# Performance work log

Measured on AMD Instinct MI355X. Metric: run time of the kernel, lower is better.

The kernel has to match this reference:

```python
import jax, jax.numpy as jnp
import numpy as np

L, B, N, IN, H, ATTN, RED, OUT = 3, 8, 512, 64, 128, 32, 32, 3


def setup_inputs() -> dict:
    key = jax.random.key(0)
    ks = jax.random.split(key, 34)
    def rn(i, shape, s=0.05):
        return jax.random.normal(ks[i], shape, dtype=jnp.float32) * s
    inp = {
        "X": rn(0, (B, N, IN), 1.0),
        # sparse binary adjacency (avg degree ~10) and denser clique graph
        "A": (jax.random.uniform(ks[1], (B, N, N)) < 0.02).astype(jnp.float32),
        "Ac": (jax.random.uniform(ks[2], (B, N, N)) < 0.05).astype(jnp.float32),
        # topo embedding
        "embed_w": rn(3, (H, IN)), "embed_b": jnp.zeros((H,), jnp.float32),
        "topo_eps": jnp.zeros((1,), jnp.float32),
        "topo_w": rn(4, (H, H)), "topo_b": jnp.zeros((H,), jnp.float32),
        "theta": rn(5, (H, 2)),
        # per-layer dual GIN (index 0: A, index 1: Ac)
        "gin_eps": jnp.zeros((L, 2, 1), jnp.float32),
        "gin_w": rn(6, (L, 2, H, H)), "gin_b": jnp.zeros((L, 2, H), jnp.float32),
        # per-layer flexible attention
        "wo": rn(7, (L, ATTN, H)), "w1": rn(8, (L, ATTN, H)),
        "wphi": rn(9, (L, ATTN)),
        "wy_w": rn(10, (L, H, H)), "wy_b": jnp.zeros((L, H), jnp.float32),
        "we_w": rn(11, (L, H, ATTN)), "we_b": jnp.zeros((L, H), jnp.float32),
        # per-layer SE block
        "lin1_w": rn(12, (L, RED, H)), "lin1_b": jnp.zeros((L, RED), jnp.float32),
        "lin2_w": rn(13, (L, H, RED)), "lin2_b": jnp.zeros((L, H), jnp.float32),
        "mlp_w": rn(14, (L, H, H)), "mlp_b": jnp.zeros((L, H), jnp.float32),
        # node head
        "head1_w": rn(15, (H // 2, H)), "head1_b": jnp.zeros((H // 2,), jnp.float32),
        "head2_w": rn(16, (OUT, H // 2)), "head2_b": jnp.zeros((OUT,), jnp.float32),
    }
    return inp


def _lin(x, w, b=None):
    y = x @ w.T
    return y if b is None else y + b


def _gin(x, a, eps, w, b):
    # (1+eps)*X + A@X, then Linear, then ReLU
    return jax.nn.relu(_lin((1.0 + eps) * x + a @ x, w, b))


def _forward(X, A, Ac, embed_w, embed_b, topo_eps, topo_w, topo_b, theta,
             gin_eps, gin_w, gin_b, wo, w1, wphi, wy_w, wy_b, we_w, we_b,
             lin1_w, lin1_b, lin2_w, lin2_b, mlp_w, mlp_b,
             head1_w, head1_b, head2_w, head2_b):
    # TopoPositionalEmbedding (shared GIN on both graphs)
    Xh = _lin(X, embed_w, embed_b)                      # (B,N,H)
    hA = _gin(Xh, A, topo_eps[0], topo_w, topo_b)
    hAC = _gin(Xh, Ac, topo_eps[0], topo_w, topo_b)
    Xp = Xh + jnp.tanh(hA * theta[:, 0]) + jnp.tanh(hAC * theta[:, 1])

    for l in range(L):
        # dual GIN
        XA = _gin(Xp, A, gin_eps[l, 0, 0], gin_w[l, 0], gin_b[l, 0])
        XAC = _gin(Xp, Ac, gin_eps[l, 1, 0], gin_w[l, 1], gin_b[l, 1])
        # GRIT-style flexible attention
        ho = Xp @ wo[l].T                               # (B,N,ATTN)
        h1 = Xp @ w1[l].T
        e = jnp.tanh(ho[:, :, None, :] + h1[:, None, :, :])   # (B,N,N,ATTN)
        alpha = jax.nn.softmax(e @ wphi[l], axis=-1)    # (B,N,N)
        Xy = _lin(Xp, wy_w[l], wy_b[l])                 # (B,N,H)
        # sum_j alpha_ij * We(e_ij) == We(sum_j alpha_ij * e_ij) since We is affine
        # and sum_j alpha_ij == 1 (avoids the (B,N,N,H) intermediate)
        ctx = jnp.einsum('bij,bijd->bid', alpha, e)     # (B,N,ATTN)
        Xatt = alpha @ Xy + _lin(ctx, we_w[l], we_b[l])
        Xbar = XA + XAC + Xatt
        # SE gating
        y1 = jax.nn.relu(_lin(Xbar.sum(axis=1), lin1_w[l], lin1_b[l]))
        y2 = jax.nn.sigmoid(_lin(y1, lin2_w[l], lin2_b[l]))
        Xp = _lin(Xbar * y2[:, None, :], mlp_w[l], mlp_b[l])

    h = jax.nn.relu(_lin(Xp, head1_w, head1_b))
    return _lin(h, head2_w, head2_b)                    # (B,N,OUT)


def reference(X, A, Ac, embed_w, embed_b, topo_eps, topo_w, topo_b, theta,
              gin_eps, gin_w, gin_b, wo, w1, wphi, wy_w, wy_b, we_w, we_b,
              lin1_w, lin1_b, lin2_w, lin2_b, mlp_w, mlp_b,
              head1_w, head1_b, head2_w, head2_b):
    return _forward(X, A, Ac, embed_w, embed_b, topo_eps, topo_w, topo_b, theta,
                    gin_eps, gin_w, gin_b, wo, w1, wphi, wy_w, wy_b, we_w, we_b,
                    lin1_w, lin1_b, lin2_w, lin2_b, mlp_w, mlp_b,
                    head1_w, head1_b, head2_w, head2_b)
```

## Files before the change

kernel.cpp:

```cpp
#include <hip/hip_runtime.h>

#define Bc 8
#define Nc 512
#define INc 64
#define Hc 128
#define Atc 32
#define REDc 32
#define OUTc 3
#define Lc 3
#define MNc (Bc * Nc)

__device__ __forceinline__ float tanh_fast(float x) {
    float e = __expf(2.f * x);
    return 1.f - 2.f * __builtin_amdgcn_rcpf(e + 1.f);
}

template <int TM, int K, int ACT>
__global__ __launch_bounds__(256) void gemm256(
        const float* __restrict__ X, const float* __restrict__ W,
        const float* __restrict__ bias, float* __restrict__ Y,
        const float* __restrict__ scale) {
    constexpr int RPG = TM / 2;
    __shared__ float xs[TM * K];
    int m0 = blockIdx.x * TM;
    int t = threadIdx.x;
    const float* sc = scale ? scale + (size_t)(m0 >> 9) * K : nullptr;
    for (int idx4 = t; idx4 < TM * K / 4; idx4 += 256) {
        float4 v = ((const float4*)(X + (size_t)m0 * K))[idx4];
        if (sc) {
            int base = idx4 * 4;
            v.x *= sc[base & (K - 1)]; v.y *= sc[(base + 1) & (K - 1)];
            v.z *= sc[(base + 2) & (K - 1)]; v.w *= sc[(base + 3) & (K - 1)];
        }
        ((float4*)xs)[idx4] = v;
    }
    __syncthreads();
    int n = t & 127;
    int grp = t >> 7;
    float bv = bias ? bias[n] : 0.f;
    float acc[RPG];
#pragma unroll
    for (int r = 0; r < RPG; ++r) acc[r] = bv;
    const float* w = W + (size_t)n * K;
    for (int k = 0; k < K; k += 4) {
        float4 wv = *(const float4*)(w + k);
#pragma unroll
        for (int r = 0; r < RPG; ++r) {
            float4 xv = *(const float4*)(xs + (grp * RPG + r) * K + k);
            acc[r] = fmaf(xv.x, wv.x, acc[r]); acc[r] = fmaf(xv.y, wv.y, acc[r]);
            acc[r] = fmaf(xv.z, wv.z, acc[r]); acc[r] = fmaf(xv.w, wv.w, acc[r]);
        }
    }
#pragma unroll
    for (int r = 0; r < RPG; ++r) {
        float v = acc[r];
        if (ACT) v = fmaxf(v, 0.f);
        Y[(size_t)(m0 + grp * RPG + r) * 128 + n] = v;
    }
}

__global__ __launch_bounds__(128) void build_csr(
        const float* __restrict__ A, const float* __restrict__ Acg,
        int* __restrict__ idxA, int* __restrict__ idxC,
        int* __restrict__ cntA, int* __restrict__ cntC) {
    int bi = blockIdx.x;
    int h = threadIdx.x;
    __shared__ int cA, cC;
    if (h == 0) { cA = 0; cC = 0; }
    __syncthreads();
    int* ia = idxA + (size_t)bi * Nc;
    int* ic = idxC + (size_t)bi * Nc;
    {
        float4 a4 = ((const float4*)(A + (size_t)bi * Nc))[h];
        if (a4.x != 0.f) ia[atomicAdd(&cA, 1)] = 4 * h;
        if (a4.y != 0.f) ia[atomicAdd(&cA, 1)] = 4 * h + 1;
        if (a4.z != 0.f) ia[atomicAdd(&cA, 1)] = 4 * h + 2;
        if (a4.w != 0.f) ia[atomicAdd(&cA, 1)] = 4 * h + 3;
        float4 c4 = ((const float4*)(Acg + (size_t)bi * Nc))[h];
        if (c4.x != 0.f) ic[atomicAdd(&cC, 1)] = 4 * h;
        if (c4.y != 0.f) ic[atomicAdd(&cC, 1)] = 4 * h + 1;
        if (c4.z != 0.f) ic[atomicAdd(&cC, 1)] = 4 * h + 2;
        if (c4.w != 0.f) ic[atomicAdd(&cC, 1)] = 4 * h + 3;
    }
    __syncthreads();
    if (h == 0) { cntA[bi] = cA; cntC[bi] = cC; }
}

__global__ __launch_bounds__(128) void spmm_pre(
        const int* __restrict__ idxA, const int* __restrict__ idxC,
        const int* __restrict__ cntA, const int* __restrict__ cntC,
        const float* __restrict__ X, const float* __restrict__ eA,
        const float* __restrict__ eC, float* __restrict__ T1, float* __restrict__ T2) {
    int bi = blockIdx.x;
    int b = bi >> 9;
    int h = threadIdx.x;
    __shared__ int ias[Nc], ics[Nc];
    int nA = cntA[bi], nC = cntC[bi];
    for (int q = h; q < nA; q += 128) ias[q] = idxA[(size_t)bi * Nc + q];
    for (int q = h; q < nC; q += 128) ics[q] = idxC[(size_t)bi * Nc + q];
    __syncthreads();
    const float* Xb = X + (size_t)b * Nc * Hc;
    float a1 = 0.f, a2 = 0.f;
    for (int q = 0; q < nA; ++q) a1 += Xb[(size_t)ias[q] * Hc + h];
    for (int q = 0; q < nC; ++q) a2 += Xb[(size_t)ics[q] * Hc + h];
    size_t o = (size_t)bi * Hc + h;
    float xv = X[o];
    T1[o] = (1.f + eA[0]) * xv + a1;
    T2[o] = (1.f + eC[0]) * xv + a2;
}

__global__ __launch_bounds__(256) void gemm2_topo(
        const float* __restrict__ T1, const float* __restrict__ T2,
        const float* __restrict__ W, const float* __restrict__ bias,
        const float* __restrict__ Xh, const float* __restrict__ theta,
        float* __restrict__ Xp) {
    __shared__ float xs1[8 * Hc], xs2[8 * Hc];
    int m0 = blockIdx.x * 8;
    int t = threadIdx.x;
    for (int idx4 = t; idx4 < 8 * Hc / 4; idx4 += 256) {
        ((float4*)xs1)[idx4] = ((const float4*)(T1 + (size_t)m0 * Hc))[idx4];
        ((float4*)xs2)[idx4] = ((const float4*)(T2 + (size_t)m0 * Hc))[idx4];
    }
    __syncthreads();
    int n = t & 127, grp = t >> 7;
    float bv = bias[n];
    float ac1[4], ac2[4];
#pragma unroll
    for (int r = 0; r < 4; ++r) { ac1[r] = bv; ac2[r] = bv; }
    const float* w = W + (size_t)n * Hc;
    for (int k = 0; k < Hc; k += 4) {
        float4 wv = *(const float4*)(w + k);
#pragma unroll
        for (int r = 0; r < 4; ++r) {
            float4 x1 = *(const float4*)(xs1 + (grp * 4 + r) * Hc + k);
            float4 x2 = *(const float4*)(xs2 + (grp * 4 + r) * Hc + k);
            ac1[r] = fmaf(x1.x, wv.x, ac1[r]); ac1[r] = fmaf(x1.y, wv.y, ac1[r]);
            ac1[r] = fmaf(x1.z, wv.z, ac1[r]); ac1[r] = fmaf(x1.w, wv.w, ac1[r]);
            ac2[r] = fmaf(x2.x, wv.x, ac2[r]); ac2[r] = fmaf(x2.y, wv.y, ac2[r]);
            ac2[r] = fmaf(x2.z, wv.z, ac2[r]); ac2[r] = fmaf(x2.w, wv.w, ac2[r]);
        }
    }
    float th0 = theta[2 * n], th1 = theta[2 * n + 1];
#pragma unroll
    for (int r = 0; r < 4; ++r) {
        size_t o = (size_t)(m0 + grp * 4 + r) * Hc + n;
        float g1 = fmaxf(ac1[r], 0.f), g2 = fmaxf(ac2[r], 0.f);
        Xp[o] = Xh[o] + tanh_fast(g1 * th0) + tanh_fast(g2 * th1);
    }
}

__global__ __launch_bounds__(256) void layer_gemms(
        const float* __restrict__ T1, const float* __restrict__ T2,
        const float* __restrict__ W1, const float* __restrict__ b1,
        const float* __restrict__ W2, const float* __restrict__ b2,
        const float* __restrict__ Xp, const float* __restrict__ wy_w,
        const float* __restrict__ wy_b, const float* __restrict__ wo,
        const float* __restrict__ w1a, float* __restrict__ GS,
        float* __restrict__ Xy, float* __restrict__ hov, float* __restrict__ h1v) {
    __shared__ float xs1[8 * Hc], xs2[8 * Hc], xs[8 * Hc];
    int m0 = blockIdx.x * 8;
    int t = threadIdx.x;
    for (int idx4 = t; idx4 < 8 * Hc / 4; idx4 += 256) {
        ((float4*)xs1)[idx4] = ((const float4*)(T1 + (size_t)m0 * Hc))[idx4];
        ((float4*)xs2)[idx4] = ((const float4*)(T2 + (size_t)m0 * Hc))[idx4];
        ((float4*)xs)[idx4]  = ((const float4*)(Xp + (size_t)m0 * Hc))[idx4];
    }
    __syncthreads();
    int n = t & 127, grp = t >> 7;
    {
        float ac1[4], ac2[4];
        float bv1 = b1[n], bv2 = b2[n];
#pragma unroll
        for (int r = 0; r < 4; ++r) { ac1[r] = bv1; ac2[r] = bv2; }
        const float* w1 = W1 + (size_t)n * Hc;
        const float* w2 = W2 + (size_t)n * Hc;
        for (int k = 0; k < Hc; k += 4) {
            float4 wv1 = *(const float4*)(w1 + k);
            float4 wv2 = *(const float4*)(w2 + k);
#pragma unroll
            for (int r = 0; r < 4; ++r) {
                float4 x1 = *(const float4*)(xs1 + (grp * 4 + r) * Hc + k);
                float4 x2 = *(const float4*)(xs2 + (grp * 4 + r) * Hc + k);
                ac1[r] = fmaf(x1.x, wv1.x, ac1[r]); ac1[r] = fmaf(x1.y, wv1.y, ac1[r]);
                ac1[r] = fmaf(x1.z, wv1.z, ac1[r]); ac1[r] = fmaf(x1.w, wv1.w, ac1[r]);
                ac2[r] = fmaf(x2.x, wv2.x, ac2[r]); ac2[r] = fmaf(x2.y, wv2.y, ac2[r]);
                ac2[r] = fmaf(x2.z, wv2.z, ac2[r]); ac2[r] = fmaf(x2.w, wv2.w, ac2[r]);
            }
        }
#pragma unroll
        for (int r = 0; r < 4; ++r) {
            size_t o = (size_t)(m0 + grp * 4 + r) * Hc + n;
            GS[o] = fmaxf(ac1[r], 0.f) + fmaxf(ac2[r], 0.f);
        }
    }
    {
        float bv = wy_b[n];
        float acc[4];
#pragma unroll
        for (int r = 0; r < 4; ++r) acc[r] = bv;
        const float* w = wy_w + (size_t)n * Hc;
        for (int k = 0; k < Hc; k += 4) {
            float4 wv = *(const float4*)(w + k);
#pragma unroll
            for (int r = 0; r < 4; ++r) {
                float4 xv = *(const float4*)(xs + (grp * 4 + r) * Hc + k);
                acc[r] = fmaf(xv.x, wv.x, acc[r]); acc[r] = fmaf(xv.y, wv.y, acc[r]);
                acc[r] = fmaf(xv.z, wv.z, acc[r]); acc[r] = fmaf(xv.w, wv.w, acc[r]);
            }
        }
#pragma unroll
        for (int r = 0; r < 4; ++r)
            Xy[(size_t)(m0 + grp * 4 + r) * Hc + n] = acc[r];
    }
    {
        int n2 = t & 63, g2 = t >> 6;
        const float* w = (n2 < 32) ? (wo + (size_t)n2 * Hc) : (w1a + (size_t)(n2 - 32) * Hc);
        float acc[2] = {0.f, 0.f};
        for (int k = 0; k < Hc; k += 4) {
            float4 wv = *(const float4*)(w + k);
#pragma unroll
            for (int r = 0; r < 2; ++r) {
                float4 xv = *(const float4*)(xs + (g2 * 2 + r) * Hc + k);
                acc[r] = fmaf(xv.x, wv.x, acc[r]); acc[r] = fmaf(xv.y, wv.y, acc[r]);
                acc[r] = fmaf(xv.z, wv.z, acc[r]); acc[r] = fmaf(xv.w, wv.w, acc[r]);
            }
        }
#pragma unroll
        for (int r = 0; r < 2; ++r) {
            int m = m0 + g2 * 2 + r;
            float v = tanh_fast(acc[r]);
            if (n2 < 32) hov[(size_t)m * Atc + n2] = v;
            else h1v[(size_t)m * Atc + (n2 - 32)] = v;
        }
    }
}

__global__ __launch_bounds__(256, 4) void attn_part(
        const float* __restrict__ ta, const float* __restrict__ tb,
        const float* __restrict__ wphi, const float* __restrict__ Xy,
        float* __restrict__ Pp, float* __restrict__ ctxp, float* __restrict__ wsp) {
    int blk = blockIdx.x;
    int b = blk >> 8;
    int r6 = (blk >> 2) & 63;
    int js = blk & 3;
    int i0 = r6 * 8;
    int t = threadIdx.x;
    __shared__ float als[8 * 128];
    __shared__ float4 red4[1024];
    __shared__ float tas[8 * 32];
    tas[t] = ta[((size_t)b * Nc + i0) * 32 + t];
    __syncthreads();
    {
        int i = t >> 5;
        int kq = t & 3;
        int jl = (t >> 2) & 7;
        float4 wp0 = ((const float4*)wphi)[kq * 2];
        float4 wp1 = ((const float4*)wphi)[kq * 2 + 1];
        float4 ta0 = *(const float4*)(tas + i * 32 + kq * 8);
        float4 ta1 = *(const float4*)(tas + i * 32 + kq * 8 + 4);
        const float* tbb = tb + ((size_t)b * Nc + js * 128) * 32;
        const float4* p = (const float4*)(tbb + (size_t)jl * 32 + kq * 8);
        float4 c0a = p[0], c0b = p[1];
        float4 c1a = p[64], c1b = p[65];
        float ca[8];
#pragma unroll
        for (int q = 0; q < 8; ++q) ca[q] = 0.f;
        float wsum = 0.f;
#pragma unroll 4
        for (int jj = 0; jj < 16; ++jj) {
            float4 ha = c0a, hb = c0b;
            c0a = c1a; c0b = c1b;
            if (jj < 14) { c1a = p[(jj + 2) * 64]; c1b = p[(jj + 2) * 64 + 1]; }
            float e0 = (ta0.x + ha.x) * __builtin_amdgcn_rcpf(fmaf(ta0.x, ha.x, 1.f));
            float e1 = (ta0.y + ha.y) * __builtin_amdgcn_rcpf(fmaf(ta0.y, ha.y, 1.f));
            float e2 = (ta0.z + ha.z) * __builtin_amdgcn_rcpf(fmaf(ta0.z, ha.z, 1.f));
            float e3 = (ta0.w + ha.w) * __builtin_amdgcn_rcpf(fmaf(ta0.w, ha.w, 1.f));
            float e4 = (ta1.x + hb.x) * __builtin_amdgcn_rcpf(fmaf(ta1.x, hb.x, 1.f));
            float e5 = (ta1.y + hb.y) * __builtin_amdgcn_rcpf(fmaf(ta1.y, hb.y, 1.f));
            float e6 = (ta1.z + hb.z) * __builtin_amdgcn_rcpf(fmaf(ta1.z, hb.z, 1.f));
            float e7 = (ta1.w + hb.w) * __builtin_amdgcn_rcpf(fmaf(ta1.w, hb.w, 1.f));
            float s01 = fmaf(e1, wp0.y, e0 * wp0.x);
            float s23 = fmaf(e3, wp0.w, e2 * wp0.z);
            float s45 = fmaf(e5, wp1.y, e4 * wp1.x);
            float s67 = fmaf(e7, wp1.w, e6 * wp1.z);
            float sc = (s01 + s23) + (s45 + s67);
            sc += __shfl_xor(sc, 1);
            sc += __shfl_xor(sc, 2);
            float w = __expf(sc);
            if (kq == 0) als[i * 128 + jj * 8 + jl] = w;
            wsum += w;
            ca[0] = fmaf(w, e0, ca[0]);
            ca[1] = fmaf(w, e1, ca[1]);
            ca[2] = fmaf(w, e2, ca[2]);
            ca[3] = fmaf(w, e3, ca[3]);
            ca[4] = fmaf(w, e4, ca[4]);
            ca[5] = fmaf(w, e5, ca[5]);
            ca[6] = fmaf(w, e6, ca[6]);
            ca[7] = fmaf(w, e7, ca[7]);
        }
#pragma unroll
        for (int o = 16; o > 0; o >>= 1) wsum += __shfl_xor(wsum, o);
        if ((t & 31) == 0) wsp[(size_t)js * MNc + (size_t)b * Nc + i0 + i] = wsum;
#pragma unroll
        for (int q = 0; q < 8; ++q) {
            ca[q] += __shfl_xor(ca[q], 4);
            ca[q] += __shfl_xor(ca[q], 8);
            ca[q] += __shfl_xor(ca[q], 16);
        }
        if (jl == 0) {
            float* cp = ctxp + ((size_t)js * MNc + (size_t)b * Nc + i0 + i) * 32 + kq * 8;
#pragma unroll
            for (int q = 0; q < 8; ++q) cp[q] = ca[q];
        }
    }
    __syncthreads();
    {
        int h4 = t & 31, jg = t >> 5;
        const float* xp = Xy + (((size_t)b * Nc + js * 128) + jg * 16) * Hc + h4 * 4;
        float* Pb = Pp + (size_t)js * MNc * Hc;
        float4 acc[8];
#pragma unroll
        for (int r = 0; r < 8; ++r) acc[r] = make_float4(0.f, 0.f, 0.f, 0.f);
        float4 xc = *(const float4*)(xp);
        float4 xn = *(const float4*)(xp + Hc);
#pragma unroll 4
        for (int jq = 0; jq < 16; ++jq) {
            float4 x = xc;
            xc = xn;
            if (jq < 14) xn = *(const float4*)(xp + (jq + 2) * Hc);
            int j = jg * 16 + jq;
#pragma unroll
            for (int r = 0; r < 8; ++r) {
                float av = als[r * 128 + j];
                acc[r].x = fmaf(av, x.x, acc[r].x);
                acc[r].y = fmaf(av, x.y, acc[r].y);
                acc[r].z = fmaf(av, x.z, acc[r].z);
                acc[r].w = fmaf(av, x.w, acc[r].w);
            }
        }
#pragma unroll
        for (int r = 0; r < 4; ++r) red4[jg * 128 + r * 32 + h4] = acc[r];
        __syncthreads();
        if (t < 128) {
            int ii = t >> 5, hq = t & 31;
            float4 s = red4[ii * 32 + hq];
#pragma unroll
            for (int gq = 1; gq < 8; ++gq) {
                float4 p = red4[gq * 128 + ii * 32 + hq];
                s.x += p.x; s.y += p.y; s.z += p.z; s.w += p.w;
            }
            *(float4*)(Pb + ((size_t)b * Nc + i0 + ii) * Hc + hq * 4) = s;
        }
        __syncthreads();
#pragma unroll
        for (int r = 0; r < 4; ++r) red4[jg * 128 + r * 32 + h4] = acc[4 + r];
        __syncthreads();
        if (t < 128) {
            int ii = t >> 5, hq = t & 31;
            float4 s = red4[ii * 32 + hq];
#pragma unroll
            for (int gq = 1; gq < 8; ++gq) {
                float4 p = red4[gq * 128 + ii * 32 + hq];
                s.x += p.x; s.y += p.y; s.z += p.z; s.w += p.w;
            }
            *(float4*)(Pb + ((size_t)b * Nc + i0 + 4 + ii) * Hc + hq * 4) = s;
        }
    }
}

__global__ __launch_bounds__(256) void combine_se(
        const float* __restrict__ Pp, const float* __restrict__ ctxp,
        const float* __restrict__ wsp, const float* __restrict__ we_w,
        const float* __restrict__ we_b, const float* __restrict__ GS,
        float* __restrict__ Xbar, float* __restrict__ part) {
    int blk = blockIdx.x;
    int m0 = blk * 8;
    int t = threadIdx.x;
    __shared__ float ctxs[8 * 32];
    __shared__ float sinv[8];
    __shared__ float4 sred[256];
    if (t < 8) {
        float ws = 0.f;
#pragma unroll
        for (int s = 0; s < 4; ++s) ws += wsp[(size_t)s * MNc + m0 + t];
        sinv[t] = 4.f / ws;
    }
    {
        float c = 0.f;
#pragma unroll
        for (int s = 0; s < 4; ++s) c += ctxp[((size_t)s * MNc + m0) * 32 + t];
        ctxs[t] = c;
    }
    __syncthreads();
    int ii = t >> 5, hq = t & 31;
    size_t o = (size_t)(m0 + ii) * Hc + hq * 4;
    float4 ps = *(const float4*)(Pp + o);
#pragma unroll
    for (int s = 1; s < 4; ++s) {
        float4 p = *(const float4*)(Pp + (size_t)s * MNc * Hc + o);
        ps.x += p.x; ps.y += p.y; ps.z += p.z; ps.w += p.w;
    }
    float si = sinv[ii];
    const float* c = ctxs + ii * 32;
    float wec[4];
#pragma unroll
    for (int ho_ = 0; ho_ < 4; ++ho_) {
        const float4* wrow = (const float4*)(we_w + (size_t)(hq * 4 + ho_) * 32);
        float sv = 0.f;
#pragma unroll
        for (int q = 0; q < 8; ++q) {
            float4 w4 = wrow[q];
            sv = fmaf(w4.x, c[4 * q], sv); sv = fmaf(w4.y, c[4 * q + 1], sv);
            sv = fmaf(w4.z, c[4 * q + 2], sv); sv = fmaf(w4.w, c[4 * q + 3], sv);
        }
        wec[ho_] = sv;
    }
    float4 wb = *(const float4*)(we_b + hq * 4);
    float4 gv = *(const float4*)(GS + o);
    float4 outv;
    outv.x = (ps.x + wec[0]) * si + wb.x + gv.x;
    outv.y = (ps.y + wec[1]) * si + wb.y + gv.y;
    outv.z = (ps.z + wec[2]) * si + wb.z + gv.z;
    outv.w = (ps.w + wec[3]) * si + wb.w + gv.w;
    *(float4*)(Xbar + o) = outv;
    sred[ii * 32 + hq] = outv;
    __syncthreads();
    if (t < 32) {
        float4 s0 = sred[t];
#pragma unroll
        for (int g = 1; g < 8; ++g) {
            float4 p = sred[g * 32 + t];
            s0.x += p.x; s0.y += p.y; s0.z += p.z; s0.w += p.w;
        }
        *(float4*)(part + (size_t)blk * Hc + t * 4) = s0;
    }
}

__global__ __launch_bounds__(256) void mlp_gemm(
        const float* __restrict__ Xbar, const float* __restrict__ W,
        const float* __restrict__ bias, const float* __restrict__ part,
        const float* __restrict__ l1w, const float* __restrict__ l1b,
        const float* __restrict__ l2w, const float* __restrict__ l2b,
        float* __restrict__ Y) {
    __shared__ float xs[8 * Hc];
    __shared__ float s[Hc];
    __shared__ float y1s[REDc];
    __shared__ float y2s[Hc];
    int m0 = blockIdx.x * 8;
    int b = m0 >> 9;
    int t = threadIdx.x;
    ((float4*)xs)[t] = ((const float4*)(Xbar + (size_t)m0 * Hc))[t];
    if (t < 128) {
        const float* pb = part + (size_t)b * 64 * Hc;
        float acc = 0.f;
        for (int p = 0; p < 64; ++p) acc += pb[p * Hc + t];
        s[t] = acc;
    }
    __syncthreads();
    if (t < REDc) {
        float a = l1b[t];
        const float* w = l1w + (size_t)t * Hc;
        for (int k = 0; k < Hc; ++k) a = fmaf(s[k], w[k], a);
        y1s[t] = fmaxf(a, 0.f);
    }
    __syncthreads();
    if (t < 128) {
        float a = l2b[t];
        const float* w2 = l2w + (size_t)t * REDc;
#pragma unroll
        for (int k = 0; k < REDc; ++k) a = fmaf(y1s[k], w2[k], a);
        y2s[t] = 1.f / (1.f + __expf(-a));
    }
    __syncthreads();
    {
        float4 yv = ((const float4*)y2s)[t & 31];
        float4 v = ((float4*)xs)[t];
        v.x *= yv.x; v.y *= yv.y; v.z *= yv.z; v.w *= yv.w;
        ((float4*)xs)[t] = v;
    }
    __syncthreads();
    int n = t & 127, grp = t >> 7;
    float bv = bias[n];
    float acc[4];
#pragma unroll
    for (int r = 0; r < 4; ++r) acc[r] = bv;
    const float* w = W + (size_t)n * Hc;
    for (int k = 0; k < Hc; k += 4) {
        float4 wv = *(const float4*)(w + k);
#pragma unroll
        for (int r = 0; r < 4; ++r) {
            float4 xv = *(const float4*)(xs + (grp * 4 + r) * Hc + k);
            acc[r] = fmaf(xv.x, wv.x, acc[r]); acc[r] = fmaf(xv.y, wv.y, acc[r]);
            acc[r] = fmaf(xv.z, wv.z, acc[r]); acc[r] = fmaf(xv.w, wv.w, acc[r]);
        }
    }
#pragma unroll
    for (int r = 0; r < 4; ++r)
        Y[(size_t)(m0 + grp * 4 + r) * Hc + n] = acc[r];
}

__global__ __launch_bounds__(256) void head_kernel(
        const float* __restrict__ Xp, const float* __restrict__ h1w,
        const float* __restrict__ h1b, const float* __restrict__ h2w,
        const float* __restrict__ h2b, float* __restrict__ out) {
    __shared__ float xs[8 * Hc];
    __shared__ float hs[8 * 64];
    int m0 = blockIdx.x * 8;
    int t = threadIdx.x;
    ((float4*)xs)[t] = ((const float4*)(Xp + (size_t)m0 * Hc))[t];
    __syncthreads();
    {
        int n = t & 63, grp = t >> 6;
        float a0 = h1b[n], a1 = a0;
        const float* w = h1w + (size_t)n * Hc;
        const float* x0 = xs + (grp * 2) * Hc;
        const float* x1 = xs + (grp * 2 + 1) * Hc;
        for (int k = 0; k < Hc; k += 4) {
            float4 wv = *(const float4*)(w + k);
            float4 v0 = *(const float4*)(x0 + k);
            float4 v1 = *(const float4*)(x1 + k);
            a0 = fmaf(v0.x, wv.x, a0); a0 = fmaf(v0.y, wv.y, a0);
            a0 = fmaf(v0.z, wv.z, a0); a0 = fmaf(v0.w, wv.w, a0);
            a1 = fmaf(v1.x, wv.x, a1); a1 = fmaf(v1.y, wv.y, a1);
            a1 = fmaf(v1.z, wv.z, a1); a1 = fmaf(v1.w, wv.w, a1);
        }
        hs[(grp * 2) * 64 + n] = fmaxf(a0, 0.f);
        hs[(grp * 2 + 1) * 64 + n] = fmaxf(a1, 0.f);
    }
    __syncthreads();
    if (t < 8 * OUTc) {
        int m = t / OUTc, o = t - m * OUTc;
        float a = h2b[o];
        const float* w2 = h2w + (size_t)o * 64;
        const float* hr = hs + m * 64;
#pragma unroll
        for (int k = 0; k < 64; ++k) a = fmaf(hr[k], w2[k], a);
        out[(size_t)(m0 + m) * OUTc + o] = a;
    }
}

extern "C" void kernel_launch(void* const* d_in, const int* in_sizes, int n_in,
                              void* d_out, int out_size, void* d_ws, size_t ws_size,
                              hipStream_t stream) {
    const float* X       = (const float*)d_in[0];
    const float* A       = (const float*)d_in[1];
    const float* Acg     = (const float*)d_in[2];
    const float* embed_w = (const float*)d_in[3];
    const float* embed_b = (const float*)d_in[4];
    const float* topo_eps= (const float*)d_in[5];
    const float* topo_w  = (const float*)d_in[6];
    const float* topo_b  = (const float*)d_in[7];
    const float* theta   = (const float*)d_in[8];
    const float* gin_eps = (const float*)d_in[9];
    const float* gin_w   = (const float*)d_in[10];
    const float* gin_b   = (const float*)d_in[11];
    const float* wo      = (const float*)d_in[12];
    const float* w1      = (const float*)d_in[13];
    const float* wphi    = (const float*)d_in[14];
    const float* wy_w    = (const float*)d_in[15];
    const float* wy_b    = (const float*)d_in[16];
    const float* we_w    = (const float*)d_in[17];
    const float* we_b    = (const float*)d_in[18];
    const float* lin1_w  = (const float*)d_in[19];
    const float* lin1_b  = (const float*)d_in[20];
    const float* lin2_w  = (const float*)d_in[21];
    const float* lin2_b  = (const float*)d_in[22];
    const float* mlp_w   = (const float*)d_in[23];
    const float* mlp_b   = (const float*)d_in[24];
    const float* head1_w = (const float*)d_in[25];
    const float* head1_b = (const float*)d_in[26];
    const float* head2_w = (const float*)d_in[27];
    const float* head2_b = (const float*)d_in[28];
    float* out = (float*)d_out;

    float* ws = (float*)d_ws;
    const int MN = Bc * Nc;
    const size_t SZ = (size_t)MN * Hc;
    float* Xh   = ws;
    float* Xp   = Xh + SZ;
    float* T1   = Xp + SZ;
    float* T2   = T1 + SZ;
    float* GS   = T2 + SZ;
    float* Xy   = GS + SZ;
    float* hov  = Xy + SZ;
    float* h1v  = hov + (size_t)MN * Atc;
    float* part = h1v + (size_t)MN * Atc;
    float* Pp   = part + (size_t)Bc * 64 * Hc;
    float* ctxp = Pp + 4 * SZ;
    float* wsp  = ctxp + (size_t)4 * MN * Atc;
    int* idxA   = (int*)(wsp + (size_t)4 * MN);
    int* idxC   = idxA + (size_t)MN * Nc;
    int* cntA   = idxC + (size_t)MN * Nc;
    int* cntC   = cntA + MN;
    float* Xbar = T1;

    build_csr<<<MN, 128, 0, stream>>>(A, Acg, idxA, idxC, cntA, cntC);
    gemm256<8, INc, 0><<<MN / 8, 256, 0, stream>>>(X, embed_w, embed_b, Xh, nullptr);
    spmm_pre<<<MN, 128, 0, stream>>>(idxA, idxC, cntA, cntC, Xh, topo_eps, topo_eps, T1, T2);
    gemm2_topo<<<MN / 8, 256, 0, stream>>>(T1, T2, topo_w, topo_b, Xh, theta, Xp);

    for (int l = 0; l < Lc; ++l) {
        spmm_pre<<<MN, 128, 0, stream>>>(idxA, idxC, cntA, cntC, Xp,
                                         gin_eps + l * 2, gin_eps + l * 2 + 1, T1, T2);
        layer_gemms<<<MN / 8, 256, 0, stream>>>(T1, T2,
            gin_w + (size_t)(l * 2 + 0) * Hc * Hc, gin_b + (size_t)(l * 2 + 0) * Hc,
            gin_w + (size_t)(l * 2 + 1) * Hc * Hc, gin_b + (size_t)(l * 2 + 1) * Hc,
            Xp, wy_w + (size_t)l * Hc * Hc, wy_b + (size_t)l * Hc,
            wo + (size_t)l * Atc * Hc, w1 + (size_t)l * Atc * Hc,
            GS, Xy, hov, h1v);
        attn_part<<<MN / 8 * 4, 256, 0, stream>>>(hov, h1v, wphi + (size_t)l * Atc, Xy,
                                                  Pp, ctxp, wsp);
        combine_se<<<MN / 8, 256, 0, stream>>>(Pp, ctxp, wsp,
                                               we_w + (size_t)l * Hc * Atc,
                                               we_b + (size_t)l * Hc, GS, Xbar, part);
        mlp_gemm<<<MN / 8, 256, 0, stream>>>(Xbar, mlp_w + (size_t)l * Hc * Hc,
                                             mlp_b + (size_t)l * Hc, part,
                                             lin1_w + (size_t)l * REDc * Hc, lin1_b + (size_t)l * REDc,
                                             lin2_w + (size_t)l * Hc * REDc, lin2_b + (size_t)l * Hc,
                                             Xp);
    }
    head_kernel<<<MN / 8, 256, 0, stream>>>(Xp, head1_w, head1_b, head2_w, head2_b, out);
}
```

Baseline: 434.6 us.

## Fuse kernels to cut launches: prologue merge, last-block combine, head into MLP

Merges CSR construction and the input embedding GEMM into one prologue launch. Folds combine_se into attn_part using a per-row-group atomic ticket, so the last of the four split blocks does the reduction and SE partial sums. Also fuses the node head into the final-layer mlp_gemm. This removes several kernel launches and intermediate round trips, at the cost of threadfence/atomic overhead and serialized tail work in the last-arriving blocks.

```diff
diff --git a/kernel.cpp b/kernel.cpp
--- a/kernel.cpp
+++ b/kernel.cpp
@@ -15,75 +15,59 @@
     return 1.f - 2.f * __builtin_amdgcn_rcpf(e + 1.f);
 }
 
-template <int TM, int K, int ACT>
-__global__ __launch_bounds__(256) void gemm256(
-        const float* __restrict__ X, const float* __restrict__ W,
-        const float* __restrict__ bias, float* __restrict__ Y,
-        const float* __restrict__ scale) {
-    constexpr int RPG = TM / 2;
-    __shared__ float xs[TM * K];
-    int m0 = blockIdx.x * TM;
-    int t = threadIdx.x;
-    const float* sc = scale ? scale + (size_t)(m0 >> 9) * K : nullptr;
-    for (int idx4 = t; idx4 < TM * K / 4; idx4 += 256) {
-        float4 v = ((const float4*)(X + (size_t)m0 * K))[idx4];
-        if (sc) {
-            int base = idx4 * 4;
-            v.x *= sc[base & (K - 1)]; v.y *= sc[(base + 1) & (K - 1)];
-            v.z *= sc[(base + 2) & (K - 1)]; v.w *= sc[(base + 3) & (K - 1)];
-        }
-        ((float4*)xs)[idx4] = v;
-    }
-    __syncthreads();
-    int n = t & 127;
-    int grp = t >> 7;
-    float bv = bias ? bias[n] : 0.f;
-    float acc[RPG];
-#pragma unroll
-    for (int r = 0; r < RPG; ++r) acc[r] = bv;
-    const float* w = W + (size_t)n * K;
-    for (int k = 0; k < K; k += 4) {
-        float4 wv = *(const float4*)(w + k);
-#pragma unroll
-        for (int r = 0; r < RPG; ++r) {
-            float4 xv = *(const float4*)(xs + (grp * RPG + r) * K + k);
-            acc[r] = fmaf(xv.x, wv.x, acc[r]); acc[r] = fmaf(xv.y, wv.y, acc[r]);
-            acc[r] = fmaf(xv.z, wv.z, acc[r]); acc[r] = fmaf(xv.w, wv.w, acc[r]);
-        }
-    }
-#pragma unroll
-    for (int r = 0; r < RPG; ++r) {
-        float v = acc[r];
-        if (ACT) v = fmaxf(v, 0.f);
-        Y[(size_t)(m0 + grp * RPG + r) * 128 + n] = v;
-    }
-}
-
-__global__ __launch_bounds__(128) void build_csr(
+__global__ __launch_bounds__(256) void prologue(
         const float* __restrict__ A, const float* __restrict__ Acg,
         int* __restrict__ idxA, int* __restrict__ idxC,
-        int* __restrict__ cntA, int* __restrict__ cntC) {
-    int bi = blockIdx.x;
-    int h = threadIdx.x;
+        int* __restrict__ cntA, int* __restrict__ cntC,
+        const float* __restrict__ X, const float* __restrict__ embed_w,
+        const float* __restrict__ embed_b, float* __restrict__ Xh) {
     __shared__ int cA, cC;
-    if (h == 0) { cA = 0; cC = 0; }
-    __syncthreads();
-    int* ia = idxA + (size_t)bi * Nc;
-    int* ic = idxC + (size_t)bi * Nc;
-    {
-        float4 a4 = ((const float4*)(A + (size_t)bi * Nc))[h];
-        if (a4.x != 0.f) ia[atomicAdd(&cA, 1)] = 4 * h;
-        if (a4.y != 0.f) ia[atomicAdd(&cA, 1)] = 4 * h + 1;
-        if (a4.z != 0.f) ia[atomicAdd(&cA, 1)] = 4 * h + 2;
-        if (a4.w != 0.f) ia[atomicAdd(&cA, 1)] = 4 * h + 3;
-        float4 c4 = ((const float4*)(Acg + (size_t)bi * Nc))[h];
-        if (c4.x != 0.f) ic[atomicAdd(&cC, 1)] = 4 * h;
-        if (c4.y != 0.f) ic[atomicAdd(&cC, 1)] = 4 * h + 1;
-        if (c4.z != 0.f) ic[atomicAdd(&cC, 1)] = 4 * h + 2;
-        if (c4.w != 0.f) ic[atomicAdd(&cC, 1)] = 4 * h + 3;
-    }
-    __syncthreads();
-    if (h == 0) { cntA[bi] = cA; cntC[bi] = cC; }
+    __shared__ float xs[8 * INc];
+    int blk = blockIdx.x;
+    int t = threadIdx.x;
+    if (blk < MNc) {
+        if (t == 0) { cA = 0; cC = 0; }
+        __syncthreads();
+        if (t < 128) {
+            int h = t;
+            int* ia = idxA + (size_t)blk * Nc;
+            int* ic = idxC + (size_t)blk * Nc;
+            float4 a4 = ((const float4*)(A + (size_t)blk * Nc))[h];
+            if (a4.x != 0.f) ia[atomicAdd(&cA, 1)] = 4 * h;
+            if (a4.y != 0.f) ia[atomicAdd(&cA, 1)] = 4 * h + 1;
+            if (a4.z != 0.f) ia[atomicAdd(&cA, 1)] = 4 * h + 2;
+            if (a4.w != 0.f) ia[atomicAdd(&cA, 1)] = 4 * h + 3;
+            float4 c4 = ((const float4*)(Acg + (size_t)blk * Nc))[h];
+            if (c4.x != 0.f) ic[atomicAdd(&cC, 1)] = 4 * h;
+            if (c4.y != 0.f) ic[atomicAdd(&cC, 1)] = 4 * h + 1;
+            if (c4.z != 0.f) ic[atomicAdd(&cC, 1)] = 4 * h + 2;
+            if (c4.w != 0.f) ic[atomicAdd(&cC, 1)] = 4 * h + 3;
+        }
+        __syncthreads();
+        if (t == 0) { cntA[blk] = cA; cntC[blk] = cC; }
+    } else {
+        int m0 = (blk - MNc) * 8;
+        if (t < 128) ((float4*)xs)[t] = ((const float4*)(X + (size_t)m0 * INc))[t];
+        __syncthreads();
+        int n = t & 127, grp = t >> 7;
+        float bv = embed_b[n];
+        float acc[4];
+#pragma unroll
+        for (int r = 0; r < 4; ++r) acc[r] = bv;
+        const float* w = embed_w + (size_t)n * INc;
+        for (int k = 0; k < INc; k += 4) {
+            float4 wv = *(const float4*)(w + k);
+#pragma unroll
+            for (int r = 0; r < 4; ++r) {
+                float4 xv = *(const float4*)(xs + (grp * 4 + r) * INc + k);
+                acc[r] = fmaf(xv.x, wv.x, acc[r]); acc[r] = fmaf(xv.y, wv.y, acc[r]);
+                acc[r] = fmaf(xv.z, wv.z, acc[r]); acc[r] = fmaf(xv.w, wv.w, acc[r]);
+            }
+        }
+#pragma unroll
+        for (int r = 0; r < 4; ++r)
+            Xh[(size_t)(m0 + grp * 4 + r) * Hc + n] = acc[r];
+    }
 }
 
 __global__ __launch_bounds__(128) void spmm_pre(
@@ -156,10 +140,12 @@
         const float* __restrict__ Xp, const float* __restrict__ wy_w,
         const float* __restrict__ wy_b, const float* __restrict__ wo,
         const float* __restrict__ w1a, float* __restrict__ GS,
-        float* __restrict__ Xy, float* __restrict__ hov, float* __restrict__ h1v) {
+        float* __restrict__ Xy, float* __restrict__ hov, float* __restrict__ h1v,
+        unsigned int* __restrict__ done) {
     __shared__ float xs1[8 * Hc], xs2[8 * Hc], xs[8 * Hc];
     int m0 = blockIdx.x * 8;
     int t = threadIdx.x;
+    if (t == 0) done[blockIdx.x] = 0u;
     for (int idx4 = t; idx4 < 8 * Hc / 4; idx4 += 256) {
         ((float4*)xs1)[idx4] = ((const float4*)(T1 + (size_t)m0 * Hc))[idx4];
         ((float4*)xs2)[idx4] = ((const float4*)(T2 + (size_t)m0 * Hc))[idx4];
@@ -238,7 +224,10 @@
 __global__ __launch_bounds__(256, 4) void attn_part(
         const float* __restrict__ ta, const float* __restrict__ tb,
         const float* __restrict__ wphi, const float* __restrict__ Xy,
-        float* __restrict__ Pp, float* __restrict__ ctxp, float* __restrict__ wsp) {
+        float* __restrict__ Pp, float* __restrict__ ctxp, float* __restrict__ wsp,
+        const float* __restrict__ we_w, const float* __restrict__ we_b,
+        const float* __restrict__ GS, float* __restrict__ Xbar,
+        float* __restrict__ part, unsigned int* __restrict__ done) {
     int blk = blockIdx.x;
     int b = blk >> 8;
     int r6 = (blk >> 2) & 63;
@@ -248,6 +237,7 @@
     __shared__ float als[8 * 128];
     __shared__ float4 red4[1024];
     __shared__ float tas[8 * 32];
+    __shared__ unsigned int ticket;
     tas[t] = ta[((size_t)b * Nc + i0) * 32 + t];
     __syncthreads();
     {
@@ -366,86 +356,90 @@
             *(float4*)(Pb + ((size_t)b * Nc + i0 + 4 + ii) * Hc + hq * 4) = s;
         }
     }
-}
-
-__global__ __launch_bounds__(256) void combine_se(
-        const float* __restrict__ Pp, const float* __restrict__ ctxp,
-        const float* __restrict__ wsp, const float* __restrict__ we_w,
-        const float* __restrict__ we_b, const float* __restrict__ GS,
-        float* __restrict__ Xbar, float* __restrict__ part) {
-    int blk = blockIdx.x;
-    int m0 = blk * 8;
-    int t = threadIdx.x;
-    __shared__ float ctxs[8 * 32];
-    __shared__ float sinv[8];
-    __shared__ float4 sred[256];
-    if (t < 8) {
-        float ws = 0.f;
-#pragma unroll
-        for (int s = 0; s < 4; ++s) ws += wsp[(size_t)s * MNc + m0 + t];
-        sinv[t] = 4.f / ws;
-    }
-    {
-        float c = 0.f;
-#pragma unroll
-        for (int s = 0; s < 4; ++s) c += ctxp[((size_t)s * MNc + m0) * 32 + t];
-        ctxs[t] = c;
-    }
-    __syncthreads();
-    int ii = t >> 5, hq = t & 31;
-    size_t o = (size_t)(m0 + ii) * Hc + hq * 4;
-    float4 ps = *(const float4*)(Pp + o);
-#pragma unroll
-    for (int s = 1; s < 4; ++s) {
-        float4 p = *(const float4*)(Pp + (size_t)s * MNc * Hc + o);
-        ps.x += p.x; ps.y += p.y; ps.z += p.z; ps.w += p.w;
-    }
-    float si = sinv[ii];
-    const float* c = ctxs + ii * 32;
-    float wec[4];
-#pragma unroll
-    for (int ho_ = 0; ho_ < 4; ++ho_) {
-        const float4* wrow = (const float4*)(we_w + (size_t)(hq * 4 + ho_) * 32);
-        float sv = 0.f;
-#pragma unroll
-        for (int q = 0; q < 8; ++q) {
-            float4 w4 = wrow[q];
-            sv = fmaf(w4.x, c[4 * q], sv); sv = fmaf(w4.y, c[4 * q + 1], sv);
-            sv = fmaf(w4.z, c[4 * q + 2], sv); sv = fmaf(w4.w, c[4 * q + 3], sv);
-        }
-        wec[ho_] = sv;
-    }
-    float4 wb = *(const float4*)(we_b + hq * 4);
-    float4 gv = *(const float4*)(GS + o);
-    float4 outv;
-    outv.x = (ps.x + wec[0]) * si + wb.x + gv.x;
-    outv.y = (ps.y + wec[1]) * si + wb.y + gv.y;
-    outv.z = (ps.z + wec[2]) * si + wb.z + gv.z;
-    outv.w = (ps.w + wec[3]) * si + wb.w + gv.w;
-    *(float4*)(Xbar + o) = outv;
-    sred[ii * 32 + hq] = outv;
-    __syncthreads();
-    if (t < 32) {
-        float4 s0 = sred[t];
-#pragma unroll
-        for (int g = 1; g < 8; ++g) {
-            float4 p = sred[g * 32 + t];
-            s0.x += p.x; s0.y += p.y; s0.z += p.z; s0.w += p.w;
-        }
-        *(float4*)(part + (size_t)blk * Hc + t * 4) = s0;
-    }
-}
-
+    __threadfence();
+    __syncthreads();
+    if (t == 0) ticket = atomicAdd(&done[blk >> 2], 1u);
+    __syncthreads();
+    if (ticket == 3u) {
+        __threadfence();
+        int rg = blk >> 2;
+        int m0c = rg * 8;
+        float* ctxs = als;
+        float* sinvs = tas;
+        float4* sred = red4;
+        if (t < 8) {
+            float wsv = 0.f;
+#pragma unroll
+            for (int s = 0; s < 4; ++s) wsv += wsp[(size_t)s * MNc + m0c + t];
+            sinvs[t] = 4.f / wsv;
+        }
+        {
+            float c = 0.f;
+#pragma unroll
+            for (int s = 0; s < 4; ++s) c += ctxp[((size_t)s * MNc + m0c) * 32 + t];
+            ctxs[t] = c;
+        }
+        __syncthreads();
+        int ii = t >> 5, hq = t & 31;
+        size_t o = (size_t)(m0c + ii) * Hc + hq * 4;
+        float4 ps = *(const float4*)(Pp + o);
+#pragma unroll
+        for (int s = 1; s < 4; ++s) {
+            float4 p = *(const float4*)(Pp + (size_t)s * MNc * Hc + o);
+            ps.x += p.x; ps.y += p.y; ps.z += p.z; ps.w += p.w;
+        }
+        float si = sinvs[ii];
+        const float* c = ctxs + ii * 32;
+        float wec[4];
+#pragma unroll
+        for (int ho_ = 0; ho_ < 4; ++ho_) {
+            const float4* wrow = (const float4*)(we_w + (size_t)(hq * 4 + ho_) * 32);
+            float sv = 0.f;
+#pragma unroll
+            for (int q = 0; q < 8; ++q) {
+                float4 w4 = wrow[q];
+                sv = fmaf(w4.x, c[4 * q], sv); sv = fmaf(w4.y, c[4 * q + 1], sv);
+                sv = fmaf(w4.z, c[4 * q + 2], sv); sv = fmaf(w4.w, c[4 * q + 3], sv);
+            }
+            wec[ho_] = sv;
+        }
+        float4 wb = *(const float4*)(we_b + hq * 4);
+        float4 gv = *(const float4*)(GS + o);
+        float4 outv;
+        outv.x = (ps.x + wec[0]) * si + wb.x + gv.x;
+        outv.y = (ps.y + wec[1]) * si + wb.y + gv.y;
+        outv.z = (ps.z + wec[2]) * si + wb.z + gv.z;
+        outv.w = (ps.w + wec[3]) * si + wb.w + gv.w;
+        *(float4*)(Xbar + o) = outv;
+        sred[ii * 32 + hq] = outv;
+        __syncthreads();
+        if (t < 32) {
+            float4 s0 = sred[t];
+#pragma unroll
+            for (int g = 1; g < 8; ++g) {
+                float4 p = sred[g * 32 + t];
+                s0.x += p.x; s0.y += p.y; s0.z += p.z; s0.w += p.w;
+            }
+            *(float4*)(part + (size_t)rg * Hc + t * 4) = s0;
+        }
+    }
+}
+
+template <int LAST>
 __global__ __launch_bounds__(256) void mlp_gemm(
         const float* __restrict__ Xbar, const float* __restrict__ W,
         const float* __restrict__ bias, const float* __restrict__ part,
         const float* __restrict__ l1w, const float* __restrict__ l1b,
         const float* __restrict__ l2w, const float* __restrict__ l2b,
-        float* __restrict__ Y) {
+        float* __restrict__ Y,
+        const float* __restrict__ h1w, const float* __restrict__ h1b,
+        const float* __restrict__ h2w, const float* __restrict__ h2b,
+        float* __restrict__ out) {
     __shared__ float xs[8 * Hc];
     __shared__ float s[Hc];
     __shared__ float y1s[REDc];
     __shared__ float y2s[Hc];
+    __shared__ float hs[8 * 64];
     int m0 = blockIdx.x * 8;
     int b = m0 >> 9;
     int t = threadIdx.x;
@@ -494,48 +488,43 @@
             acc[r] = fmaf(xv.z, wv.z, acc[r]); acc[r] = fmaf(xv.w, wv.w, acc[r]);
         }
     }
-#pragma unroll
-    for (int r = 0; r < 4; ++r)
-        Y[(size_t)(m0 + grp * 4 + r) * Hc + n] = acc[r];
-}
-
-__global__ __launch_bounds__(256) void head_kernel(
-        const float* __restrict__ Xp, const float* __restrict__ h1w,
-        const float* __restrict__ h1b, const float* __restrict__ h2w,
-        const float* __restrict__ h2b, float* __restrict__ out) {
-    __shared__ float xs[8 * Hc];
-    __shared__ float hs[8 * 64];
-    int m0 = blockIdx.x * 8;
-    int t = threadIdx.x;
-    ((float4*)xs)[t] = ((const float4*)(Xp + (size_t)m0 * Hc))[t];
-    __syncthreads();
-    {
-        int n = t & 63, grp = t >> 6;
-        float a0 = h1b[n], a1 = a0;
-        const float* w = h1w + (size_t)n * Hc;
-        const float* x0 = xs + (grp * 2) * Hc;
-        const float* x1 = xs + (grp * 2 + 1) * Hc;
-        for (int k = 0; k < Hc; k += 4) {
-            float4 wv = *(const float4*)(w + k);
-            float4 v0 = *(const float4*)(x0 + k);
-            float4 v1 = *(const float4*)(x1 + k);
-            a0 = fmaf(v0.x, wv.x, a0); a0 = fmaf(v0.y, wv.y, a0);
-            a0 = fmaf(v0.z, wv.z, a0); a0 = fmaf(v0.w, wv.w, a0);
-            a1 = fmaf(v1.x, wv.x, a1); a1 = fmaf(v1.y, wv.y, a1);
-            a1 = fmaf(v1.z, wv.z, a1); a1 = fmaf(v1.w, wv.w, a1);
-        }
-        hs[(grp * 2) * 64 + n] = fmaxf(a0, 0.f);
-        hs[(grp * 2 + 1) * 64 + n] = fmaxf(a1, 0.f);
-    }
-    __syncthreads();
-    if (t < 8 * OUTc) {
-        int m = t / OUTc, o = t - m * OUTc;
-        float a = h2b[o];
-        const float* w2 = h2w + (size_t)o * 64;
-        const float* hr = hs + m * 64;
-#pragma unroll
-        for (int k = 0; k < 64; ++k) a = fmaf(hr[k], w2[k], a);
-        out[(size_t)(m0 + m) * OUTc + o] = a;
+    if (!LAST) {
+#pragma unroll
+        for (int r = 0; r < 4; ++r)
+            Y[(size_t)(m0 + grp * 4 + r) * Hc + n] = acc[r];
+    } else {
+        __syncthreads();
+#pragma unroll
+        for (int r = 0; r < 4; ++r) xs[(grp * 4 + r) * Hc + n] = acc[r];
+        __syncthreads();
+        {
+            int n2 = t & 63, g2 = t >> 6;
+            float a0 = h1b[n2], a1 = a0;
+            const float* wh = h1w + (size_t)n2 * Hc;
+            const float* x0 = xs + (g2 * 2) * Hc;
+            const float* x1 = xs + (g2 * 2 + 1) * Hc;
+            for (int k = 0; k < Hc; k += 4) {
+                float4 wv = *(const float4*)(wh + k);
+                float4 v0 = *(const float4*)(x0 + k);
+                float4 v1 = *(const float4*)(x1 + k);
+                a0 = fmaf(v0.x, wv.x, a0); a0 = fmaf(v0.y, wv.y, a0);
+                a0 = fmaf(v0.z, wv.z, a0); a0 = fmaf(v0.w, wv.w, a0);
+                a1 = fmaf(v1.x, wv.x, a1); a1 = fmaf(v1.y, wv.y, a1);
+                a1 = fmaf(v1.z, wv.z, a1); a1 = fmaf(v1.w, wv.w, a1);
+            }
+            hs[(g2 * 2) * 64 + n2] = fmaxf(a0, 0.f);
+            hs[(g2 * 2 + 1) * 64 + n2] = fmaxf(a1, 0.f);
+        }
+        __syncthreads();
+        if (t < 8 * OUTc) {
+            int m = t / OUTc, o = t - m * OUTc;
+            float a = h2b[o];
+            const float* w2 = h2w + (size_t)o * 64;
+            const float* hr = hs + m * 64;
+#pragma unroll
+            for (int k = 0; k < 64; ++k) a = fmaf(hr[k], w2[k], a);
+            out[(size_t)(m0 + m) * OUTc + o] = a;
+        }
     }
 }
 
@@ -585,17 +574,18 @@
     float* hov  = Xy + SZ;
     float* h1v  = hov + (size_t)MN * Atc;
     float* part = h1v + (size_t)MN * Atc;
-    float* Pp   = part + (size_t)Bc * 64 * Hc;
+    float* Pp   = part + (size_t)(MN / 8) * Hc;
     float* ctxp = Pp + 4 * SZ;
     float* wsp  = ctxp + (size_t)4 * MN * Atc;
     int* idxA   = (int*)(wsp + (size_t)4 * MN);
     int* idxC   = idxA + (size_t)MN * Nc;
     int* cntA   = idxC + (size_t)MN * Nc;
     int* cntC   = cntA + MN;
+    unsigned int* done = (unsigned int*)(cntC + MN);
     float* Xbar = T1;
 
-    build_csr<<<MN, 128, 0, stream>>>(A, Acg, idxA, idxC, cntA, cntC);
-    gemm256<8, INc, 0><<<MN / 8, 256, 0, stream>>>(X, embed_w, embed_b, Xh, nullptr);
+    prologue<<<MN + MN / 8, 256, 0, stream>>>(A, Acg, idxA, idxC, cntA, cntC,
+                                              X, embed_w, embed_b, Xh);
     spmm_pre<<<MN, 128, 0, stream>>>(idxA, idxC, cntA, cntC, Xh, topo_eps, topo_eps, T1, T2);
     gemm2_topo<<<MN / 8, 256, 0, stream>>>(T1, T2, topo_w, topo_b, Xh, theta, Xp);
 
@@ -607,17 +597,23 @@
             gin_w + (size_t)(l * 2 + 1) * Hc * Hc, gin_b + (size_t)(l * 2 + 1) * Hc,
             Xp, wy_w + (size_t)l * Hc * Hc, wy_b + (size_t)l * Hc,
             wo + (size_t)l * Atc * Hc, w1 + (size_t)l * Atc * Hc,
-            GS, Xy, hov, h1v);
-        attn_part<<<MN / 8 * 4, 256, 0, stream>>>(hov, h1v, wphi + (size_t)l * Atc, Xy,
-                                                  Pp, ctxp, wsp);
-        combine_se<<<MN / 8, 256, 0, stream>>>(Pp, ctxp, wsp,
-                                               we_w + (size_t)l * Hc * Atc,
-                                               we_b + (size_t)l * Hc, GS, Xbar, part);
-        mlp_gemm<<<MN / 8, 256, 0, stream>>>(Xbar, mlp_w + (size_t)l * Hc * Hc,
-                                             mlp_b + (size_t)l * Hc, part,
-                                             lin1_w + (size_t)l * REDc * Hc, lin1_b + (size_t)l * REDc,
-                                             lin2_w + (size_t)l * Hc * REDc, lin2_b + (size_t)l * Hc,
-                                             Xp);
-    }
-    head_kernel<<<MN / 8, 256, 0, stream>>>(Xp, head1_w, head1_b, head2_w, head2_b, out);
-}
+            GS, Xy, hov, h1v, done);
+        attn_part<<<MN / 2, 256, 0, stream>>>(hov, h1v, wphi + (size_t)l * Atc, Xy,
+                                              Pp, ctxp, wsp,
+                                              we_w + (size_t)l * Hc * Atc,
+                                              we_b + (size_t)l * Hc, GS, Xbar, part, done);
+        if (l < Lc - 1) {
+            mlp_gemm<0><<<MN / 8, 256, 0, stream>>>(Xbar, mlp_w + (size_t)l * Hc * Hc,
+                mlp_b + (size_t)l * Hc, part,
+                lin1_w + (size_t)l * REDc * Hc, lin1_b + (size_t)l * REDc,
+                lin2_w + (size_t)l * Hc * REDc, lin2_b + (size_t)l * Hc,
+                Xp, head1_w, head1_b, head2_w, head2_b, out);
+        } else {
+            mlp_gemm<1><<<MN / 8, 256, 0, stream>>>(Xbar, mlp_w + (size_t)l * Hc * Hc,
+                mlp_b + (size_t)l * Hc, part,
+                lin1_w + (size_t)l * REDc * Hc, lin1_b + (size_t)l * REDc,
+                lin2_w + (size_t)l * Hc * REDc, lin2_b + (size_t)l * Hc,
+                Xp, head1_w, head1_b, head2_w, head2_b, out);
+        }
+    }
+}
```

New measurement: 1.337 ms. 208% more time.
